# Kernel optimization log

Hardware: AMD Instinct MI355X
Metric: run time of the kernel (lower is better)

## Reference

```python
import math
import jax, jax.numpy as jnp
import numpy as np

B, CI, CO, K, WD, H = 8, 512, 512, 3, 512, 64


def setup_inputs() -> dict:
    key = jax.random.key(0)
    ks = jax.random.split(key, 8)
    x = jax.random.normal(ks[0], (B, CI, H, H), jnp.float32)
    style = jax.random.normal(ks[1], (B, WD), jnp.float32)
    noise = jax.random.normal(ks[2], (B, CO, H, H), jnp.float32)
    # learned params
    weight = jax.random.normal(ks[3], (1, CO, CI, K, K), jnp.float32)      # ModulatedConv2d.weight
    mod_weight = jax.random.normal(ks[4], (CI, WD), jnp.float32)            # EqualLinear.weight
    mod_bias = jnp.ones((CI,), jnp.float32)                                  # bias_init=1
    noise_weight = 0.1 * jnp.ones((1,), jnp.float32)                         # NoiseInjection.weight (nonzero for signal)
    act_bias = 0.01 * jax.random.normal(ks[5], (CO,), jnp.float32)           # FusedLeakyReLU.bias
    return {"x": x, "style": style, "noise": noise, "weight": weight,
            "mod_weight": mod_weight, "mod_bias": mod_bias,
            "noise_weight": noise_weight, "act_bias": act_bias}


def reference(x, style, noise, weight, mod_weight, mod_bias, noise_weight, act_bias):
    # EqualLinear modulation: scale = 1/sqrt(w_space_dim), lr_mul = 1
    eq_scale = 1.0 / math.sqrt(WD)
    s = style @ (mod_weight * eq_scale).T + mod_bias            # [B, CI]
    # modulate + demodulate per-sample weights
    conv_scale = 1.0 / math.sqrt(CI * K * K)                     # 1/sqrt(fan_in)
    w = conv_scale * weight * s[:, None, :, None, None]          # [B, CO, CI, K, K]
    demod = jax.lax.rsqrt(jnp.sum(w * w, axis=(2, 3, 4)) + 1e-8)  # [B, CO]
    w = w * demod[:, :, None, None, None]
    pad = K // 2

    def conv1(xi, wi):  # per-sample conv (equivalent to groups=batch trick)
        return jax.lax.conv_general_dilated(
            xi[None], wi, window_strides=(1, 1),
            padding=[(pad, pad), (pad, pad)],
            dimension_numbers=("NCHW", "OIHW", "NCHW"))[0]

    out = jax.vmap(conv1)(x, w)                                  # [B, CO, H, H]
    # noise injection (noise provided -> no normalization branch)
    out = out + noise_weight[0] * noise
    # fused leaky relu: leaky_relu(out + bias) * sqrt(2)
    out = jax.nn.leaky_relu(out + act_bias[None, :, None, None], 0.2) * math.sqrt(2.0)
    return out
```

## Files before the change

### kernel.cpp

```cpp
#include <hip/hip_runtime.h>
#include <hip/hip_bf16.h>

typedef unsigned short u16;
typedef unsigned long long u64;
typedef short bf16x8 __attribute__((ext_vector_type(8)));
typedef float f32x4 __attribute__((ext_vector_type(4)));

#define EQ_SCALE   0.04419417382415922f
#define CONV_SCALE 0.014731391274719738f

#define WS_S   0
#define WS_ESC (16*1024)
#define WS_WSQ (32*1024)
#define WS_WT  (32*1024 + 1024*1024)
#define WS_XS  (WS_WT + 9*512*512*2)
#define WS_Z   (WS_XS + 8*64*64*512*2)

__device__ __forceinline__ void gld16(void* l, const void* g) {
  __builtin_amdgcn_global_load_lds((const __attribute__((address_space(1))) void*)g,
                                   (__attribute__((address_space(3))) void*)l,
                                   16, 0, 0);
}

__device__ __forceinline__ u16 f2b_rne(float f) {
  union { float f; unsigned int i; } c; c.f = f;
  unsigned int r = (c.i + 0x7FFFu + ((c.i >> 16) & 1u)) >> 16;
  return (u16)r;
}

__global__ void __launch_bounds__(256) k_pre1(
    const float* __restrict__ style, const float* __restrict__ mw,
    const float* __restrict__ mb, const float* __restrict__ w,
    float* __restrict__ s, float* __restrict__ wsq, u64* __restrict__ z) {
  int bid = blockIdx.x, t = threadIdx.x;
  if (bid < 32) { z[bid * 256 + t] = 0ull; return; }
  if (bid < 1056) {
    int idx = (bid - 32) * 256 + t;
    const float* p = w + idx * 9;
    float a = 0.f;
#pragma unroll
    for (int k = 0; k < 9; ++k) { float v = p[k]; a += v * v; }
    wsq[idx] = a;
    return;
  }
  int g = (bid - 1056) * 4 + (t >> 6);
  int lane = t & 63;
  int b = g >> 9, i = g & 511;
  const float4* sr = (const float4*)(style + (b << 9));
  const float4* wr = (const float4*)(mw + (i << 9));
  float acc = 0.f;
#pragma unroll
  for (int j = 0; j < 2; ++j) {
    float4 a4 = sr[lane * 2 + j];
    float4 w4 = wr[lane * 2 + j];
    acc += a4.x * w4.x + a4.y * w4.y + a4.z * w4.z + a4.w * w4.w;
  }
#pragma unroll
  for (int off = 32; off; off >>= 1) acc += __shfl_xor(acc, off);
  if (lane == 0) s[g] = acc * EQ_SCALE + mb[i];
}

__global__ void __launch_bounds__(256) k_pre2(
    const float* __restrict__ wsq, const float* __restrict__ s,
    const float* __restrict__ w, const float* __restrict__ x,
    float* __restrict__ esc, u16* __restrict__ wt, u16* __restrict__ xs) {
  __shared__ u16 tile[64 * 66];
  int bid = blockIdx.x, t = threadIdx.x;
  if (bid < 1024) {
    int g = bid * 4 + (t >> 6);
    int lane = t & 63;
    int b = g >> 9, o = g & 511;
    const float4* wr = (const float4*)(wsq + (o << 9));
    const float4* sr = (const float4*)(s + (b << 9));
    float a = 0.f;
#pragma unroll
    for (int j = 0; j < 2; ++j) {
      float4 wv = wr[lane * 2 + j];
      float4 sv = sr[lane * 2 + j];
      a += wv.x*sv.x*sv.x + wv.y*sv.y*sv.y + wv.z*sv.z*sv.z + wv.w*sv.w*sv.w;
    }
#pragma unroll
    for (int off = 32; off; off >>= 1) a += __shfl_xor(a, off);
    if (lane == 0) esc[g] = CONV_SCALE * rsqrtf(CONV_SCALE * CONV_SCALE * a + 1e-8f);
    return;
  }
  if (bid < 2048) {
    int idx = (bid - 1024) * 256 + t;
    const float* p = w + idx * 9;
#pragma unroll
    for (int k = 0; k < 9; ++k) wt[k * 262144 + idx] = f2b_rne(p[k]);
    return;
  }
  int v = bid - 2048;
  int by = v & 511, i0 = (v >> 9) << 6;
  int b = by >> 6, y = by & 63;
  int wv = t >> 6, lane = t & 63;
  for (int k = 0; k < 16; ++k) {
    int il = wv + (k << 2);
    int i = i0 + il;
    float val = x[((((b << 9) + i) << 6) | y) << 6 | lane] * s[(b << 9) + i];
    tile[lane * 66 + il] = f2b_rne(val);
  }
  __syncthreads();
  for (int k = 0; k < 16; ++k) {
    int xc = wv + (k << 2);
    xs[((((b << 6) | y) << 6 | xc) << 9) + i0 + lane] = tile[xc * 66 + lane];
  }
}

__global__ void __launch_bounds__(512, 1) k_conv(
    const u16* __restrict__ wt, const u16* __restrict__ xs,
    const u16* __restrict__ zbuf,
    const float* __restrict__ esc, const float* __restrict__ noise,
    const float* __restrict__ nwp, const float* __restrict__ abias,
    float* __restrict__ out) {
  __shared__ __align__(16) u16 ldsA[2][256 * 64];
  __shared__ __align__(16) u16 ldsB[2][384 * 64];

  const int t = threadIdx.x;
  const int w = t >> 6, lane = t & 63;
  const int wm = w >> 2, wrw = w & 3;
  const int quad = lane >> 4, l15 = lane & 15;

  const int flat = blockIdx.y * 2 + blockIdx.x;
  const int xcd = flat & 7, rest = flat >> 3;
  const int o0 = (xcd >> 2) << 8;
  const int nt = (rest << 2) | (xcd & 3);
  const int b = nt >> 4, y0 = (nt & 15) << 2;

  const u16* bgp[6];
#pragma unroll
  for (int j = 0; j < 6; ++j) {
    int c = j * 512 + t;
    int pos = c >> 3, swz = c & 7;
    int ci16 = swz ^ (pos & 7);
    int col = pos & 63;
    int yy = y0 - 1 + j;
    if ((unsigned)yy < 64u)
      bgp[j] = xs + ((((b << 6) + yy) << 6) + col) * 512 + ci16 * 8;
    else
      bgp[j] = zbuf + col * 512 + ci16 * 8;
  }
  int agOff[4];
#pragma unroll
  for (int j = 0; j < 4; ++j) {
    int c = j * 512 + t;
    int ol = c >> 3, swz = c & 7;
    int ci16 = swz ^ (ol & 7);
    agOff[j] = (o0 + ol) * 512 + ci16 * 8;
  }

  f32x4 acc[32];
#pragma unroll
  for (int i = 0; i < 32; ++i) acc[i] = (f32x4)0.f;

  const int aBase0 = wm * 1024 + l15 * 8;
  const int aXorS = l15 & 7;

#pragma unroll
  for (int j = 0; j < 6; ++j)
    gld16(&ldsB[0][(j * 512 + w * 64) * 8], bgp[j]);
#pragma unroll
  for (int j = 0; j < 4; ++j)
    gld16(&ldsA[0][(j * 512 + w * 64) * 8], wt + agOff[j]);

#pragma unroll 1
  for (int cib = 0; cib < 8; ++cib) {
    const u16* bR = &ldsB[cib & 1][0];
#pragma unroll
    for (int khw = 0; khw < 9; ++khw) {
      if (khw == 7) { asm volatile("s_waitcnt vmcnt(6)" ::: "memory"); }
      else         { asm volatile("s_waitcnt vmcnt(0)" ::: "memory"); }
      __builtin_amdgcn_s_barrier();
      __builtin_amdgcn_sched_barrier(0);

      const int par = (cib + khw) & 1;
      const u16* aR = &ldsA[par][0];

      {
        u16* aW = (u16*)&ldsA[par ^ 1][0];
        const int nkhw = (khw == 8) ? 0 : khw + 1;
        const int ncib = (khw == 8) ? ((cib + 1) & 7) : cib;
#pragma unroll
        for (int j = 0; j < 4; ++j)
          gld16(aW + (j * 512 + w * 64) * 8,
                wt + agOff[j] + nkhw * 262144 + ncib * 64);
      }
      if (khw == 6) {
        u16* bW = (u16*)&ldsB[(cib & 1) ^ 1][0];
        const int pc = (cib + 1) & 7;
#pragma unroll
        for (int j = 0; j < 6; ++j)
          gld16(bW + (j * 512 + w * 64) * 8, bgp[j] + pc * 64);
      }

      const int kh = khw / 3, kw = khw % 3;
      const int tr = wrw + kh;
      int bBase[4], bXor[4];
      unsigned cmask[4];
#pragma unroll
      for (int nf = 0; nf < 4; ++nf) {
        int ci = nf * 16 + l15 + kw - 1;
        cmask[nf] = ((kw == 0 && nf == 0) || (kw == 2 && nf == 3))
                        ? (unsigned)((unsigned)ci > 63u) : 0u;
        ci &= 63;
        int pos = tr * 64 + ci;
        bBase[nf] = pos * 8;
        bXor[nf] = pos & 7;
      }
#pragma unroll
      for (int ks = 0; ks < 2; ++ks) {
        const int kci = ks * 4 + quad;
        bf16x8 af[8], bv[4];
#pragma unroll
        for (int mf = 0; mf < 8; ++mf)
          af[mf] = *(const bf16x8*)(aR + (aBase0 + mf * 128 + (kci ^ aXorS)) * 8);
#pragma unroll
        for (int nf = 0; nf < 4; ++nf) {
          bf16x8 v = *(const bf16x8*)(bR + (bBase[nf] + (kci ^ bXor[nf])) * 8);
          bf16x8 z = {0, 0, 0, 0, 0, 0, 0, 0};
          bv[nf] = cmask[nf] ? z : v;
        }
        __builtin_amdgcn_s_setprio(1);
#pragma unroll
        for (int mf = 0; mf < 8; ++mf)
#pragma unroll
          for (int nf = 0; nf < 4; ++nf)
            acc[mf * 4 + nf] = __builtin_amdgcn_mfma_f32_16x16x32_bf16(
                af[mf], bv[nf], acc[mf * 4 + nf], 0, 0, 0);
        __builtin_amdgcn_s_setprio(0);
      }
    }
  }
  asm volatile("s_waitcnt vmcnt(0)" ::: "memory");

  const float nwv = nwp[0];
  const int y = y0 + wrw;
#pragma unroll
  for (int mf = 0; mf < 8; ++mf) {
#pragma unroll
    for (int r = 0; r < 4; ++r) {
      int o = o0 + wm * 128 + mf * 16 + quad * 4 + r;
      float es = esc[(b << 9) + o];
      float ab = abias[o];
      int rowbase = ((((b << 9) + o) << 6) | y) << 6;
#pragma unroll
      for (int nf = 0; nf < 4; ++nf) {
        int col = nf * 16 + l15;
        int idx = rowbase | col;
        float v = acc[mf * 4 + nf][r] * es + nwv * noise[idx] + ab;
        v = (v < 0.f ? 0.2f * v : v) * 1.4142135623730951f;
        out[idx] = v;
      }
    }
  }
}

extern "C" void kernel_launch(void* const* d_in, const int* in_sizes, int n_in,
                              void* d_out, int out_size, void* d_ws, size_t ws_size,
                              hipStream_t stream) {
  const float* x      = (const float*)d_in[0];
  const float* style  = (const float*)d_in[1];
  const float* noise  = (const float*)d_in[2];
  const float* weight = (const float*)d_in[3];
  const float* mw     = (const float*)d_in[4];
  const float* mb     = (const float*)d_in[5];
  const float* nw     = (const float*)d_in[6];
  const float* ab     = (const float*)d_in[7];
  float* out = (float*)d_out;

  char* ws = (char*)d_ws;
  float* s   = (float*)(ws + WS_S);
  float* esc = (float*)(ws + WS_ESC);
  float* wsq = (float*)(ws + WS_WSQ);
  u16* wt    = (u16*)(ws + WS_WT);
  u16* xs    = (u16*)(ws + WS_XS);
  u16* zbuf  = (u16*)(ws + WS_Z);

  k_pre1<<<2080, 256, 0, stream>>>(style, mw, mb, weight, s, wsq, (u64*)zbuf);
  k_pre2<<<6144, 256, 0, stream>>>(wsq, s, weight, x, esc, wt, xs);
  k_conv<<<dim3(2, 128), 512, 0, stream>>>(wt, xs, zbuf, esc, noise, nw, ab, out);
}
```

Baseline: 353.1 us.

## Double conv threads per block, split K-steps with interleaved prefetch and barriers

The conv kernel moves from 512 to 1024 threads per block. Each wave now owns 64 output channels instead of 128, which halves the accumulator registers per thread. Global-to-LDS prefetches are split across the two K sub-steps and placed between extra barriers so they overlap MFMA work. The zero-row buffer is addressed through an offset from xs, and the pre-kernel transpose store is vectorized to 4-element writes. The extra barriers and the larger block add synchronization cost.

Measured after the change: 391.3 us. 1.11x slower.

```diff
diff --git a/kernel.cpp b/kernel.cpp
--- a/kernel.cpp
+++ b/kernel.cpp
@@ -102,15 +102,20 @@
     tile[lane * 66 + il] = f2b_rne(val);
   }
   __syncthreads();
-  for (int k = 0; k < 16; ++k) {
-    int xc = wv + (k << 2);
-    xs[((((b << 6) | y) << 6 | xc) << 9) + i0 + lane] = tile[xc * 66 + lane];
-  }
-}
-
-__global__ void __launch_bounds__(512, 1) k_conv(
+  int row = t >> 4, qt = t & 15;
+  for (int k = 0; k < 4; ++k) {
+    int xc = row + k * 16;
+    short4 o4;
+    o4.x = (short)tile[xc * 66 + qt * 4 + 0];
+    o4.y = (short)tile[xc * 66 + qt * 4 + 1];
+    o4.z = (short)tile[xc * 66 + qt * 4 + 2];
+    o4.w = (short)tile[xc * 66 + qt * 4 + 3];
+    *(short4*)(&xs[((((b << 6) | y) << 6 | xc) << 9) + i0 + qt * 4]) = o4;
+  }
+}
+
+__global__ void __launch_bounds__(1024) k_conv(
     const u16* __restrict__ wt, const u16* __restrict__ xs,
-    const u16* __restrict__ zbuf,
     const float* __restrict__ esc, const float* __restrict__ noise,
     const float* __restrict__ nwp, const float* __restrict__ abias,
     float* __restrict__ out) {
@@ -119,7 +124,7 @@
 
   const int t = threadIdx.x;
   const int w = t >> 6, lane = t & 63;
-  const int wm = w >> 2, wrw = w & 3;
+  const int og = w >> 2, wrw = w & 3;
   const int quad = lane >> 4, l15 = lane & 15;
 
   const int flat = blockIdx.y * 2 + blockIdx.x;
@@ -128,71 +133,57 @@
   const int nt = (rest << 2) | (xcd & 3);
   const int b = nt >> 4, y0 = (nt & 15) << 2;
 
-  const u16* bgp[6];
-#pragma unroll
-  for (int j = 0; j < 6; ++j) {
-    int c = j * 512 + t;
+  int bgOff[3];
+#pragma unroll
+  for (int j = 0; j < 3; ++j) {
+    int c = j * 1024 + t;
     int pos = c >> 3, swz = c & 7;
     int ci16 = swz ^ (pos & 7);
-    int col = pos & 63;
-    int yy = y0 - 1 + j;
+    int tr = pos >> 6, col = pos & 63;
+    int yy = y0 - 1 + tr;
     if ((unsigned)yy < 64u)
-      bgp[j] = xs + ((((b << 6) + yy) << 6) + col) * 512 + ci16 * 8;
+      bgOff[j] = ((((b << 6) + yy) << 6) + col) * 512 + ci16 * 8;
     else
-      bgp[j] = zbuf + col * 512 + ci16 * 8;
-  }
-  int agOff[4];
-#pragma unroll
-  for (int j = 0; j < 4; ++j) {
-    int c = j * 512 + t;
+      bgOff[j] = 8 * 64 * 64 * 512 + col * 512 + ci16 * 8;
+  }
+  int agOff[2];
+#pragma unroll
+  for (int j = 0; j < 2; ++j) {
+    int c = j * 1024 + t;
     int ol = c >> 3, swz = c & 7;
     int ci16 = swz ^ (ol & 7);
     agOff[j] = (o0 + ol) * 512 + ci16 * 8;
   }
 
-  f32x4 acc[32];
-#pragma unroll
-  for (int i = 0; i < 32; ++i) acc[i] = (f32x4)0.f;
-
-  const int aBase0 = wm * 1024 + l15 * 8;
+  f32x4 acc[16];
+#pragma unroll
+  for (int i = 0; i < 16; ++i) acc[i] = (f32x4)0.f;
+
+  const int aB0 = og * 512 + l15 * 8;
   const int aXorS = l15 & 7;
 
 #pragma unroll
-  for (int j = 0; j < 6; ++j)
-    gld16(&ldsB[0][(j * 512 + w * 64) * 8], bgp[j]);
-#pragma unroll
-  for (int j = 0; j < 4; ++j)
-    gld16(&ldsA[0][(j * 512 + w * 64) * 8], wt + agOff[j]);
+  for (int j = 0; j < 3; ++j)
+    gld16(&ldsB[0][(j * 1024 + w * 64) * 8], xs + bgOff[j]);
+#pragma unroll
+  for (int j = 0; j < 2; ++j)
+    gld16(&ldsA[0][(j * 1024 + w * 64) * 8], wt + agOff[j]);
 
 #pragma unroll 1
   for (int cib = 0; cib < 8; ++cib) {
     const u16* bR = &ldsB[cib & 1][0];
 #pragma unroll
     for (int khw = 0; khw < 9; ++khw) {
-      if (khw == 7) { asm volatile("s_waitcnt vmcnt(6)" ::: "memory"); }
-      else         { asm volatile("s_waitcnt vmcnt(0)" ::: "memory"); }
+      if (khw == 7) { asm volatile("s_waitcnt vmcnt(3)" ::: "memory"); }
+      else          { asm volatile("s_waitcnt vmcnt(0)" ::: "memory"); }
       __builtin_amdgcn_s_barrier();
       __builtin_amdgcn_sched_barrier(0);
 
       const int par = (cib + khw) & 1;
       const u16* aR = &ldsA[par][0];
-
-      {
-        u16* aW = (u16*)&ldsA[par ^ 1][0];
-        const int nkhw = (khw == 8) ? 0 : khw + 1;
-        const int ncib = (khw == 8) ? ((cib + 1) & 7) : cib;
-#pragma unroll
-        for (int j = 0; j < 4; ++j)
-          gld16(aW + (j * 512 + w * 64) * 8,
-                wt + agOff[j] + nkhw * 262144 + ncib * 64);
-      }
-      if (khw == 6) {
-        u16* bW = (u16*)&ldsB[(cib & 1) ^ 1][0];
-        const int pc = (cib + 1) & 7;
-#pragma unroll
-        for (int j = 0; j < 6; ++j)
-          gld16(bW + (j * 512 + w * 64) * 8, bgp[j] + pc * 64);
-      }
+      u16* aW = (u16*)&ldsA[par ^ 1][0];
+      const int nkhw = (khw == 8) ? 0 : khw + 1;
+      const int ncib = (khw == 8) ? ((cib + 1) & 7) : cib;
 
       const int kh = khw / 3, kw = khw % 3;
       const int tr = wrw + kh;
@@ -204,32 +195,64 @@
         cmask[nf] = ((kw == 0 && nf == 0) || (kw == 2 && nf == 3))
                         ? (unsigned)((unsigned)ci > 63u) : 0u;
         ci &= 63;
-        int pos = tr * 64 + ci;
-        bBase[nf] = pos * 8;
-        bXor[nf] = pos & 7;
-      }
-#pragma unroll
-      for (int ks = 0; ks < 2; ++ks) {
-        const int kci = ks * 4 + quad;
-        bf16x8 af[8], bv[4];
-#pragma unroll
-        for (int mf = 0; mf < 8; ++mf)
-          af[mf] = *(const bf16x8*)(aR + (aBase0 + mf * 128 + (kci ^ aXorS)) * 8);
+        bBase[nf] = (tr * 64 + ci) * 8;
+        bXor[nf] = ci & 7;
+      }
+
+      bf16x8 af0[4], bv0[4];
+      {
+        const int kci = quad;
+#pragma unroll
+        for (int mf = 0; mf < 4; ++mf)
+          af0[mf] = *(const bf16x8*)(aR + (aB0 + mf * 128 + (kci ^ aXorS)) * 8);
 #pragma unroll
         for (int nf = 0; nf < 4; ++nf) {
           bf16x8 v = *(const bf16x8*)(bR + (bBase[nf] + (kci ^ bXor[nf])) * 8);
           bf16x8 z = {0, 0, 0, 0, 0, 0, 0, 0};
-          bv[nf] = cmask[nf] ? z : v;
+          bv0[nf] = cmask[nf] ? z : v;
         }
-        __builtin_amdgcn_s_setprio(1);
-#pragma unroll
-        for (int mf = 0; mf < 8; ++mf)
-#pragma unroll
-          for (int nf = 0; nf < 4; ++nf)
-            acc[mf * 4 + nf] = __builtin_amdgcn_mfma_f32_16x16x32_bf16(
-                af[mf], bv[nf], acc[mf * 4 + nf], 0, 0, 0);
-        __builtin_amdgcn_s_setprio(0);
-      }
+      }
+      gld16(aW + (0 * 1024 + w * 64) * 8, wt + agOff[0] + nkhw * 262144 + ncib * 64);
+      __builtin_amdgcn_s_barrier();
+      __builtin_amdgcn_s_setprio(1);
+#pragma unroll
+      for (int mf = 0; mf < 4; ++mf)
+#pragma unroll
+        for (int nf = 0; nf < 4; ++nf)
+          acc[mf * 4 + nf] = __builtin_amdgcn_mfma_f32_16x16x32_bf16(
+              af0[mf], bv0[nf], acc[mf * 4 + nf], 0, 0, 0);
+      __builtin_amdgcn_s_setprio(0);
+
+      bf16x8 af1[4], bv1[4];
+      {
+        const int kci = 4 + quad;
+#pragma unroll
+        for (int mf = 0; mf < 4; ++mf)
+          af1[mf] = *(const bf16x8*)(aR + (aB0 + mf * 128 + (kci ^ aXorS)) * 8);
+#pragma unroll
+        for (int nf = 0; nf < 4; ++nf) {
+          bf16x8 v = *(const bf16x8*)(bR + (bBase[nf] + (kci ^ bXor[nf])) * 8);
+          bf16x8 z = {0, 0, 0, 0, 0, 0, 0, 0};
+          bv1[nf] = cmask[nf] ? z : v;
+        }
+      }
+      gld16(aW + (1 * 1024 + w * 64) * 8, wt + agOff[1] + nkhw * 262144 + ncib * 64);
+      if (khw == 6) {
+        u16* bW = (u16*)&ldsB[(cib & 1) ^ 1][0];
+        const int pc = (cib + 1) & 7;
+#pragma unroll
+        for (int j = 0; j < 3; ++j)
+          gld16(bW + (j * 1024 + w * 64) * 8, xs + bgOff[j] + pc * 64);
+      }
+      __builtin_amdgcn_s_barrier();
+      __builtin_amdgcn_s_setprio(1);
+#pragma unroll
+      for (int mf = 0; mf < 4; ++mf)
+#pragma unroll
+        for (int nf = 0; nf < 4; ++nf)
+          acc[mf * 4 + nf] = __builtin_amdgcn_mfma_f32_16x16x32_bf16(
+              af1[mf], bv1[nf], acc[mf * 4 + nf], 0, 0, 0);
+      __builtin_amdgcn_s_setprio(0);
     }
   }
   asm volatile("s_waitcnt vmcnt(0)" ::: "memory");
@@ -237,10 +260,10 @@
   const float nwv = nwp[0];
   const int y = y0 + wrw;
 #pragma unroll
-  for (int mf = 0; mf < 8; ++mf) {
+  for (int mf = 0; mf < 4; ++mf) {
 #pragma unroll
     for (int r = 0; r < 4; ++r) {
-      int o = o0 + wm * 128 + mf * 16 + quad * 4 + r;
+      int o = o0 + og * 64 + mf * 16 + quad * 4 + r;
       float es = esc[(b << 9) + o];
       float ab = abias[o];
       int rowbase = ((((b << 9) + o) << 6) | y) << 6;
@@ -279,5 +302,5 @@
 
   k_pre1<<<2080, 256, 0, stream>>>(style, mw, mb, weight, s, wsq, (u64*)zbuf);
   k_pre2<<<6144, 256, 0, stream>>>(wsq, s, weight, x, esc, wt, xs);
-  k_conv<<<dim3(2, 128), 512, 0, stream>>>(wt, xs, zbuf, esc, noise, nw, ab, out);
-}
+  k_conv<<<dim3(2, 128), 1024, 0, stream>>>(wt, xs, esc, noise, nw, ab, out);
+}
```

## Split conv k-step into four interleaved phases with staggered global-to-LDS loads

Applied to the files above, without the earlier changes.

Restructures the conv main loop so each 3x3 tap runs as four MFMA phases (half of M by half of K). Each phase has its own LDS fragment reads, and the next stage's weight and input loads are spread one chunk per phase. It adds barriers between phases and sets waves_per_eu to 2, aiming for finer overlap of memory traffic with MFMA work and lower register pressure. It also vectorises the transpose store in the prep kernel to 4-wide shorts. The risks are barrier overhead and subtle LDS write-after-read hazards from the tighter double-buffer schedule.

After: 364.4 us. 1.03x slower.

```diff
diff --git a/kernel.cpp b/kernel.cpp
--- a/kernel.cpp
+++ b/kernel.cpp
@@ -102,13 +102,20 @@
     tile[lane * 66 + il] = f2b_rne(val);
   }
   __syncthreads();
-  for (int k = 0; k < 16; ++k) {
-    int xc = wv + (k << 2);
-    xs[((((b << 6) | y) << 6 | xc) << 9) + i0 + lane] = tile[xc * 66 + lane];
-  }
-}
-
-__global__ void __launch_bounds__(512, 1) k_conv(
+  int row = t >> 4, qt = t & 15;
+  for (int k = 0; k < 4; ++k) {
+    int xc = row + k * 16;
+    short4 o4;
+    o4.x = (short)tile[xc * 66 + qt * 4 + 0];
+    o4.y = (short)tile[xc * 66 + qt * 4 + 1];
+    o4.z = (short)tile[xc * 66 + qt * 4 + 2];
+    o4.w = (short)tile[xc * 66 + qt * 4 + 3];
+    *(short4*)(&xs[((((b << 6) | y) << 6 | xc) << 9) + i0 + qt * 4]) = o4;
+  }
+}
+
+__attribute__((amdgpu_waves_per_eu(2, 2)))
+__global__ void __launch_bounds__(512) k_conv(
     const u16* __restrict__ wt, const u16* __restrict__ xs,
     const u16* __restrict__ zbuf,
     const float* __restrict__ esc, const float* __restrict__ noise,
@@ -154,7 +161,7 @@
 #pragma unroll
   for (int i = 0; i < 32; ++i) acc[i] = (f32x4)0.f;
 
-  const int aBase0 = wm * 1024 + l15 * 8;
+  const int aB0 = wm * 1024 + l15 * 8;
   const int aXorS = l15 & 7;
 
 #pragma unroll
@@ -163,36 +170,20 @@
 #pragma unroll
   for (int j = 0; j < 4; ++j)
     gld16(&ldsA[0][(j * 512 + w * 64) * 8], wt + agOff[j]);
+  asm volatile("s_waitcnt vmcnt(0)" ::: "memory");
+  __builtin_amdgcn_s_barrier();
 
 #pragma unroll 1
   for (int cib = 0; cib < 8; ++cib) {
     const u16* bR = &ldsB[cib & 1][0];
 #pragma unroll
     for (int khw = 0; khw < 9; ++khw) {
-      if (khw == 7) { asm volatile("s_waitcnt vmcnt(6)" ::: "memory"); }
-      else         { asm volatile("s_waitcnt vmcnt(0)" ::: "memory"); }
-      __builtin_amdgcn_s_barrier();
-      __builtin_amdgcn_sched_barrier(0);
-
       const int par = (cib + khw) & 1;
       const u16* aR = &ldsA[par][0];
-
-      {
-        u16* aW = (u16*)&ldsA[par ^ 1][0];
-        const int nkhw = (khw == 8) ? 0 : khw + 1;
-        const int ncib = (khw == 8) ? ((cib + 1) & 7) : cib;
-#pragma unroll
-        for (int j = 0; j < 4; ++j)
-          gld16(aW + (j * 512 + w * 64) * 8,
-                wt + agOff[j] + nkhw * 262144 + ncib * 64);
-      }
-      if (khw == 6) {
-        u16* bW = (u16*)&ldsB[(cib & 1) ^ 1][0];
-        const int pc = (cib + 1) & 7;
-#pragma unroll
-        for (int j = 0; j < 6; ++j)
-          gld16(bW + (j * 512 + w * 64) * 8, bgp[j] + pc * 64);
-      }
+      u16* aW = (u16*)&ldsA[par ^ 1][0];
+      const int nkhw = (khw == 8) ? 0 : khw + 1;
+      const int ncib = (khw == 8) ? ((cib + 1) & 7) : cib;
+      const int aStageOff = nkhw * 262144 + ncib * 64;
 
       const int kh = khw / 3, kw = khw % 3;
       const int tr = wrw + kh;
@@ -204,32 +195,106 @@
         cmask[nf] = ((kw == 0 && nf == 0) || (kw == 2 && nf == 3))
                         ? (unsigned)((unsigned)ci > 63u) : 0u;
         ci &= 63;
-        int pos = tr * 64 + ci;
-        bBase[nf] = pos * 8;
-        bXor[nf] = pos & 7;
-      }
-#pragma unroll
-      for (int ks = 0; ks < 2; ++ks) {
-        const int kci = ks * 4 + quad;
-        bf16x8 af[8], bv[4];
-#pragma unroll
-        for (int mf = 0; mf < 8; ++mf)
-          af[mf] = *(const bf16x8*)(aR + (aBase0 + mf * 128 + (kci ^ aXorS)) * 8);
-#pragma unroll
-        for (int nf = 0; nf < 4; ++nf) {
-          bf16x8 v = *(const bf16x8*)(bR + (bBase[nf] + (kci ^ bXor[nf])) * 8);
-          bf16x8 z = {0, 0, 0, 0, 0, 0, 0, 0};
-          bv[nf] = cmask[nf] ? z : v;
-        }
-        __builtin_amdgcn_s_setprio(1);
-#pragma unroll
-        for (int mf = 0; mf < 8; ++mf)
-#pragma unroll
-          for (int nf = 0; nf < 4; ++nf)
-            acc[mf * 4 + nf] = __builtin_amdgcn_mfma_f32_16x16x32_bf16(
-                af[mf], bv[nf], acc[mf * 4 + nf], 0, 0, 0);
-        __builtin_amdgcn_s_setprio(0);
-      }
+        bBase[nf] = (tr * 64 + ci) * 8;
+        bXor[nf] = ci & 7;
+      }
+      const bf16x8 zf = {0, 0, 0, 0, 0, 0, 0, 0};
+
+      bf16x8 af[4], bv0[4], bv1[4];
+
+#pragma unroll
+      for (int m = 0; m < 4; ++m)
+        af[m] = *(const bf16x8*)(aR + (aB0 + m * 128 + (quad ^ aXorS)) * 8);
+#pragma unroll
+      for (int nf = 0; nf < 4; ++nf) {
+        bf16x8 v = *(const bf16x8*)(bR + (bBase[nf] + (quad ^ bXor[nf])) * 8);
+        bv0[nf] = cmask[nf] ? zf : v;
+      }
+      gld16(aW + (0 * 512 + w * 64) * 8, wt + agOff[0] + aStageOff);
+      __builtin_amdgcn_s_barrier();
+      asm volatile("s_waitcnt lgkmcnt(0)" ::: "memory");
+      __builtin_amdgcn_sched_barrier(0);
+      __builtin_amdgcn_s_setprio(1);
+#pragma unroll
+      for (int m = 0; m < 4; ++m)
+#pragma unroll
+        for (int nf = 0; nf < 4; ++nf)
+          acc[m * 4 + nf] = __builtin_amdgcn_mfma_f32_16x16x32_bf16(
+              af[m], bv0[nf], acc[m * 4 + nf], 0, 0, 0);
+      __builtin_amdgcn_s_setprio(0);
+      __builtin_amdgcn_s_barrier();
+
+#pragma unroll
+      for (int m = 0; m < 4; ++m)
+        af[m] = *(const bf16x8*)(aR + (aB0 + (m + 4) * 128 + (quad ^ aXorS)) * 8);
+#pragma unroll
+      for (int nf = 0; nf < 4; ++nf) {
+        bf16x8 v = *(const bf16x8*)(bR + (bBase[nf] + ((4 + quad) ^ bXor[nf])) * 8);
+        bv1[nf] = cmask[nf] ? zf : v;
+      }
+      gld16(aW + (1 * 512 + w * 64) * 8, wt + agOff[1] + aStageOff);
+      __builtin_amdgcn_s_barrier();
+      asm volatile("s_waitcnt lgkmcnt(0)" ::: "memory");
+      __builtin_amdgcn_sched_barrier(0);
+      __builtin_amdgcn_s_setprio(1);
+#pragma unroll
+      for (int m = 0; m < 4; ++m)
+#pragma unroll
+        for (int nf = 0; nf < 4; ++nf)
+          acc[(m + 4) * 4 + nf] = __builtin_amdgcn_mfma_f32_16x16x32_bf16(
+              af[m], bv0[nf], acc[(m + 4) * 4 + nf], 0, 0, 0);
+      __builtin_amdgcn_s_setprio(0);
+      __builtin_amdgcn_s_barrier();
+
+#pragma unroll
+      for (int m = 0; m < 4; ++m)
+        af[m] = *(const bf16x8*)(aR + (aB0 + m * 128 + ((4 + quad) ^ aXorS)) * 8);
+      gld16(aW + (2 * 512 + w * 64) * 8, wt + agOff[2] + aStageOff);
+      if (khw == 6) {
+        u16* bW = (u16*)&ldsB[(cib & 1) ^ 1][0];
+        const int pc = (cib + 1) & 7;
+#pragma unroll
+        for (int j = 0; j < 3; ++j)
+          gld16(bW + (j * 512 + w * 64) * 8, bgp[j] + pc * 64);
+      }
+      __builtin_amdgcn_s_barrier();
+      asm volatile("s_waitcnt lgkmcnt(0)" ::: "memory");
+      __builtin_amdgcn_sched_barrier(0);
+      __builtin_amdgcn_s_setprio(1);
+#pragma unroll
+      for (int m = 0; m < 4; ++m)
+#pragma unroll
+        for (int nf = 0; nf < 4; ++nf)
+          acc[m * 4 + nf] = __builtin_amdgcn_mfma_f32_16x16x32_bf16(
+              af[m], bv1[nf], acc[m * 4 + nf], 0, 0, 0);
+      __builtin_amdgcn_s_setprio(0);
+      __builtin_amdgcn_s_barrier();
+
+#pragma unroll
+      for (int m = 0; m < 4; ++m)
+        af[m] = *(const bf16x8*)(aR + (aB0 + (m + 4) * 128 + ((4 + quad) ^ aXorS)) * 8);
+      gld16(aW + (3 * 512 + w * 64) * 8, wt + agOff[3] + aStageOff);
+      if (khw == 6) {
+        u16* bW = (u16*)&ldsB[(cib & 1) ^ 1][0];
+        const int pc = (cib + 1) & 7;
+#pragma unroll
+        for (int j = 3; j < 6; ++j)
+          gld16(bW + (j * 512 + w * 64) * 8, bgp[j] + pc * 64);
+      }
+      __builtin_amdgcn_s_barrier();
+      asm volatile("s_waitcnt lgkmcnt(0)" ::: "memory");
+      __builtin_amdgcn_sched_barrier(0);
+      __builtin_amdgcn_s_setprio(1);
+#pragma unroll
+      for (int m = 0; m < 4; ++m)
+#pragma unroll
+        for (int nf = 0; nf < 4; ++nf)
+          acc[(m + 4) * 4 + nf] = __builtin_amdgcn_mfma_f32_16x16x32_bf16(
+              af[m], bv1[nf], acc[(m + 4) * 4 + nf], 0, 0, 0);
+      __builtin_amdgcn_s_setprio(0);
+      if (khw == 6) { asm volatile("s_waitcnt vmcnt(3)" ::: "memory"); }
+      else          { asm volatile("s_waitcnt vmcnt(0)" ::: "memory"); }
+      __builtin_amdgcn_s_barrier();
     }
   }
   asm volatile("s_waitcnt vmcnt(0)" ::: "memory");
```
